# Performance work log

Measured on AMD Instinct MI355X. Metric: run time of the kernel, lower is better.

The kernel has to match this reference:

```python
import jax, jax.numpy as jnp
import numpy as np

HEADS = 8
DIM_HEAD = 64
NB_FEATURES = 256
CHUNK = 128          # chunk size used by performer's causal_linear_attention_noncuda
EPS_KERNEL = 1e-4    # eps in softmax_kernel feature map
EPS_DENOM = 1e-6     # eps added to k_cumsum in the denominator


def softmax_kernel(data, proj, is_query):
    # FAVOR+ positive softmax random features (performer_pytorch.softmax_kernel)
    # data: [B,H,N,D], proj: [M,D]
    d = data.shape[-1]
    normalizer = d ** -0.25
    ratio = proj.shape[0] ** -0.5
    data_dash = jnp.einsum('bhnd,md->bhnm', data * normalizer, proj)
    # ||x||^2 / (2*sqrt(d))
    diag = jnp.sum(data * data, axis=-1, keepdims=True) * 0.5 * (normalizer ** 2)
    if is_query:
        m = jax.lax.stop_gradient(jnp.max(data_dash, axis=-1, keepdims=True))
    else:
        m = jax.lax.stop_gradient(jnp.max(data_dash, axis=(-1, -2), keepdims=True))
    return ratio * (jnp.exp(data_dash - diag - m) + EPS_KERNEL)


def causal_linear_attention(qp, kp, v, chunk=CHUNK):
    # Chunked causal linear attention (O(N) in seq len):
    # out_i = q'_i . S_i / (q'_i . z_i), S_i = sum_{j<=i} k'_j v_j^T, z_i = cumsum k'_j
    B, H, N, M = qp.shape
    E = v.shape[-1]
    C = N // chunk

    def to_chunks(x):
        return x.reshape(B, H, C, chunk, x.shape[-1]).transpose(2, 0, 1, 3, 4)

    qc, kc, vc = to_chunks(qp), to_chunks(kp), to_chunks(v)
    k0 = jnp.zeros((B, H, M), qp.dtype)
    s0 = jnp.zeros((B, H, M, E), qp.dtype)

    def step(carry, inp):
        k_last, s_last = carry
        q, k, vv = inp  # [B,H,c,M], [B,H,c,M], [B,H,c,E]
        k_cum = k_last[:, :, None, :] + jnp.cumsum(k, axis=2)           # [B,H,c,M]
        d_inv = 1.0 / jnp.einsum('bhnm,bhnm->bhn', q, k_cum + EPS_DENOM)
        ctx = jnp.einsum('bhnm,bhne->bhnme', k, vv)                      # [B,H,c,M,E]
        s_cum = s_last[:, :, None] + jnp.cumsum(ctx, axis=2)             # [B,H,c,M,E]
        out = jnp.einsum('bhnme,bhnm,bhn->bhne', s_cum, q, d_inv)        # [B,H,c,E]
        return (k_cum[:, :, -1, :], s_cum[:, :, -1]), out

    _, outs = jax.lax.scan(step, (k0, s0), (qc, kc, vc))  # [C,B,H,c,E]
    return outs.transpose(1, 2, 0, 3, 4).reshape(B, H, N, E)


def setup_inputs() -> dict:
    key = jax.random.key(0)
    k1, k2, k3, k4 = jax.random.split(key, 4)
    B, N, D = 4, 2048, 512
    return {
        'query': jax.random.normal(k1, (B, N, D), jnp.float32),
        'key': jax.random.normal(k2, (B, N, D), jnp.float32),
        'value': jax.random.normal(k3, (B, N, D), jnp.float32),
        'projection': jax.random.normal(k4, (NB_FEATURES, DIM_HEAD), jnp.float32),
    }


def reference(query, key, value, projection):
    B, N, D = query.shape

    def split(x):  # [B,N,D] -> [B,H,N,Dh]
        return x.reshape(B, N, HEADS, DIM_HEAD).transpose(0, 2, 1, 3)

    q, k, v = split(query), split(key), split(value)
    qp = softmax_kernel(q, projection, is_query=True)
    kp = softmax_kernel(k, projection, is_query=False)
    out = causal_linear_attention(qp, kp, v)
    return out.transpose(0, 2, 1, 3).reshape(B, N, D)
```

## Files before the change

### kernel.cpp

```cpp
#include <hip/hip_runtime.h>
#include <math.h>

#define BB 4
#define NN 2048
#define DD 512
#define HH 8
#define DH 64
#define MM 256
#define BH 32
#define CHK 128
#define NCH 16
#define ROWS (BH*NN)

constexpr float NRM   = 0.35355339059327373f;
constexpr float RATIO = 0.0625f;
constexpr float EPSK  = 1e-4f;
constexpr float EPSD  = 1e-6f;
constexpr float REPS  = 0.0625f * 1e-4f;

#define OFFB_QP   ((size_t)0)
#define OFFB_SP   ((size_t)33554432)
#define OFFB_KP   (OFFB_SP + (size_t)16777216)
#define OFFB_VT   (OFFB_KP + (size_t)33554432)
#define OFFB_Z    (OFFB_VT + (size_t)8388608)
#define OFFB_KMP  (OFFB_Z  + (size_t)524288)
#define OFFB_SF   (OFFB_KMP + (size_t)4096)
#define OFFB_PJB  (OFFB_SF + (size_t)4096)

typedef __attribute__((ext_vector_type(8))) short short8;
typedef __attribute__((ext_vector_type(4))) float f32x4;

__device__ __forceinline__ float b2f(ushort u) {
  union { float f; unsigned int i; } x; x.i = ((unsigned int)u) << 16; return x.f;
}
__device__ __forceinline__ ushort f2b(float f) {
  unsigned int u = __float_as_uint(f);
  unsigned int r = (u + 0x7FFFu + ((u >> 16) & 1u)) >> 16;
  return (ushort)r;
}

#define MFMA(a,b,c) __builtin_amdgcn_mfma_f32_16x16x32_bf16(a, b, c, 0, 0, 0)

__global__ __launch_bounds__(256) void prep_kernel(const float* __restrict__ proj,
                                                   char* __restrict__ ws) {
  const int i = blockIdx.x*256 + threadIdx.x;
  float4 v = *(const float4*)(proj + (size_t)i*4);
  ushort4 o;
  o.x = f2b(v.x); o.y = f2b(v.y); o.z = f2b(v.z); o.w = f2b(v.w);
  *(ushort4*)((ushort*)(ws + OFFB_PJB) + (size_t)i*4) = o;
}

template<int MODE>
__device__ __forceinline__ void featm_body(const float* __restrict__ inp,
                                           const ushort* __restrict__ projb,
                                           char* __restrict__ ws,
                                           char* lds, int blk) {
  ushort* xh = (ushort*)lds;
  ushort* xl = xh + 64*72;
  ushort* ps = xl + 64*72;
  ushort* qt = (ushort*)lds;
  float* diag_s = (float*)(lds + 36864);
  float (*wmax)[4] = (float(*)[4])(lds + 37120);
  float* kred = (float*)(lds + 38144);

  const int t  = threadIdx.x;
  const int w  = t >> 6;
  const int l  = t & 63;
  const int lq = l >> 4;
  const int ln = l & 15;

  const int rowbase = blk * 64;
  const int bh = rowbase >> 11;
  const int b  = bh >> 3, h = bh & 7;
  const int n0 = rowbase & (NN - 1);

  {
    const int r  = t >> 2;
    const int c0 = (t & 3) * 16;
    const float* src = inp + ((size_t)(b*NN + n0 + r))*DD + h*DH + c0;
    float vv[16];
    #pragma unroll
    for (int j = 0; j < 4; ++j) {
      float4 v = *(const float4*)(src + j*4);
      vv[4*j+0] = v.x*NRM; vv[4*j+1] = v.y*NRM;
      vv[4*j+2] = v.z*NRM; vv[4*j+3] = v.w*NRM;
    }
    float s = 0.f;
    ushort hi[16], lo[16];
    #pragma unroll
    for (int j = 0; j < 16; ++j) {
      s += vv[j]*vv[j];
      hi[j] = f2b(vv[j]);
      lo[j] = f2b(vv[j] - b2f(hi[j]));
    }
    *(short8*)(xh + r*72 + c0)     = *(short8*)&hi[0];
    *(short8*)(xh + r*72 + c0 + 8) = *(short8*)&hi[8];
    *(short8*)(xl + r*72 + c0)     = *(short8*)&lo[0];
    *(short8*)(xl + r*72 + c0 + 8) = *(short8*)&lo[8];
    s += __shfl_xor(s, 1); s += __shfl_xor(s, 2);
    if ((t & 3) == 0) diag_s[r] = 0.5f * s;
  }

  f32x4 acc[4][4];
  #pragma unroll
  for (int mt = 0; mt < 4; ++mt)
    #pragma unroll
    for (int c = 0; c < 4; ++c) acc[mt][c] = (f32x4){0.f,0.f,0.f,0.f};

  #pragma unroll
  for (int p = 0; p < 2; ++p) {
    if (p) __syncthreads();
    #pragma unroll
    for (int ld = 0; ld < 4; ++ld) {
      int flat = t + 256*ld;
      int r = flat >> 3, g = flat & 7;
      *(short8*)(ps + r*72 + g*8) = *(const short8*)(projb + (size_t)(p*128 + r)*DH + g*8);
    }
    __syncthreads();
    #pragma unroll
    for (int kk = 0; kk < 2; ++kk) {
      short8 ah[4], al[4];
      #pragma unroll
      for (int mt = 0; mt < 4; ++mt) {
        ah[mt] = *(const short8*)(xh + (mt*16 + ln)*72 + kk*32 + lq*8);
        al[mt] = *(const short8*)(xl + (mt*16 + ln)*72 + kk*32 + lq*8);
      }
      #pragma unroll
      for (int ntl = 0; ntl < 2; ++ntl) {
        short8 bf = *(const short8*)(ps + (w*32 + ntl*16 + ln)*72 + kk*32 + lq*8);
        #pragma unroll
        for (int mt = 0; mt < 4; ++mt) {
          acc[mt][2*p+ntl] = MFMA(al[mt], bf, acc[mt][2*p+ntl]);
          acc[mt][2*p+ntl] = MFMA(ah[mt], bf, acc[mt][2*p+ntl]);
        }
      }
    }
  }

  if (MODE == 0) {
    #pragma unroll
    for (int mt = 0; mt < 4; ++mt)
      #pragma unroll
      for (int reg = 0; reg < 4; ++reg) {
        float m = acc[mt][0][reg];
        #pragma unroll
        for (int c = 1; c < 4; ++c) m = fmaxf(m, acc[mt][c][reg]);
        m = fmaxf(m, __shfl_xor(m, 1));
        m = fmaxf(m, __shfl_xor(m, 2));
        m = fmaxf(m, __shfl_xor(m, 4));
        m = fmaxf(m, __shfl_xor(m, 8));
        if (ln == 0) wmax[mt*16 + lq*4 + reg][w] = m;
      }
  } else {
    float mx = -1e30f;
    #pragma unroll
    for (int mt = 0; mt < 4; ++mt)
      #pragma unroll
      for (int c = 0; c < 4; ++c)
        #pragma unroll
        for (int reg = 0; reg < 4; ++reg) mx = fmaxf(mx, acc[mt][c][reg]);
    #pragma unroll
    for (int m = 1; m < 64; m <<= 1) mx = fmaxf(mx, __shfl_xor(mx, m));
    if (l == 0) kred[w] = mx;
  }
  __syncthreads();

  float km = 0.f;
  if (MODE == 1) {
    km = fmaxf(fmaxf(kred[0], kred[1]), fmaxf(kred[2], kred[3]));
    if (t == 0) ((float*)(ws + OFFB_KMP))[blk] = km;
  }

  #pragma unroll
  for (int mt = 0; mt < 4; ++mt)
    #pragma unroll
    for (int reg = 0; reg < 4; ++reg) {
      const int row = mt*16 + lq*4 + reg;
      float rm;
      if (MODE == 0) {
        float4 wm4 = *(const float4*)&wmax[row][0];
        rm = fmaxf(fmaxf(wm4.x, wm4.y), fmaxf(wm4.z, wm4.w));
      } else {
        rm = km;
      }
      const float dg = diag_s[row];
      #pragma unroll
      for (int c = 0; c < 4; ++c) {
        const int f = (c >> 1)*128 + w*32 + (c & 1)*16 + ln;
        const float e = __expf(acc[mt][c][reg] - dg - rm);
        qt[row*264 + f] = f2b(MODE == 0 ? RATIO*(e + EPSK) : e);
      }
    }
  __syncthreads();

  ushort* dstbase = (ushort*)(ws + (MODE == 0 ? OFFB_QP : OFFB_KP)) + (size_t)rowbase*MM;
  #pragma unroll
  for (int ld = 0; ld < 8; ++ld) {
    int flat = t + 256*ld;
    int row = flat >> 5, g = flat & 31;
    *(short8*)(dstbase + (size_t)row*MM + g*8) = *(const short8*)(qt + row*264 + g*8);
  }
}

__device__ __forceinline__ void vt_body(const float* __restrict__ value,
                                        char* __restrict__ ws,
                                        char* lds, int blk) {
  float (*vsh)[68] = (float(*)[68])lds;
  const int t = threadIdx.x;
  const int bh = blk >> 4, nc = blk & 15;
  const int b = bh >> 3, h = bh & 7;
  const int n0 = nc * CHK;
  #pragma unroll
  for (int l = 0; l < 8; ++l) {
    int flat = t + 256*l;
    int r = flat >> 4, g = flat & 15;
    *(float4*)&vsh[r][g*4] = *(const float4*)(value + ((size_t)(b*NN + n0 + r))*DD + h*DH + g*4);
  }
  __syncthreads();
  const int e = t & 63, qd = t >> 6;
  ushort* vt = (ushort*)(ws + OFFB_VT) + ((size_t)bh*DH + e)*NN + n0 + qd*32;
  #pragma unroll
  for (int p = 0; p < 16; ++p) {
    unsigned int lo = f2b(vsh[qd*32 + 2*p][e]);
    unsigned int hi = f2b(vsh[qd*32 + 2*p + 1][e]);
    ((unsigned int*)vt)[p] = lo | (hi << 16);
  }
}

__global__ __launch_bounds__(256) void mega_kernel(const float* __restrict__ q,
                                                   const float* __restrict__ k,
                                                   const float* __restrict__ v,
                                                   char* __restrict__ ws) {
  __shared__ __align__(16) char lds[38160];
  const ushort* projb = (const ushort*)(ws + OFFB_PJB);
  const int blk = blockIdx.x;
  if (blk < 1024)       featm_body<0>(q, projb, ws, lds, blk);
  else if (blk < 2048)  featm_body<1>(k, projb, ws, lds, blk - 1024);
  else                  vt_body(v, ws, lds, blk - 2048);
}

__global__ __launch_bounds__(256) void sfac_kernel(char* __restrict__ ws) {
  const int blk = blockIdx.x*256 + threadIdx.x;
  const int bh = blk >> 5;
  const float* kmp = (const float*)(ws + OFFB_KMP);
  float km = -1e30f;
  #pragma unroll
  for (int i = 0; i < 32; ++i) km = fmaxf(km, kmp[bh*32 + i]);
  ((float*)(ws + OFFB_SF))[blk] = RATIO * __expf(kmp[blk] - km);
}

__global__ __launch_bounds__(256) void sprefix_kernel(char* __restrict__ ws) {
  __shared__ __align__(16) unsigned int kpTu[16*68];
  __shared__ __align__(16) ushort Vts[64*136];
  __shared__ float zred[16][16];

  const int t  = threadIdx.x;
  const int w  = t >> 6;
  const int l  = t & 63;
  const int lq = l >> 4;
  const int ln = l & 15;
  const int bh = blockIdx.x >> 4;
  const int ms = blockIdx.x & 15;

  const ushort* kpb = (const ushort*)(ws + OFFB_KP) + (size_t)bh*NN*MM + ms*16;
  const ushort* vtb = (const ushort*)(ws + OFFB_VT) + (size_t)bh*DH*NN;
  const float*  sf  = (const float*)(ws + OFFB_SF);
  ushort* spb = (ushort*)(ws + OFFB_SP) + (size_t)bh*NCH*DH*MM + ms*16;
  float*  zb  = (float*)(ws + OFFB_Z) + (size_t)bh*NCH*MM + ms*16;

  f32x4 acc = (f32x4){0.f,0.f,0.f,0.f};
  float zrun = 0.f;

  for (int tc = 0; tc < NCH; ++tc) {
    __syncthreads();

    if (t < 16) {
      if (tc > 0) {
        float s = 0.f;
        #pragma unroll
        for (int q = 0; q < 16; ++q) s += zred[q][t];
        zrun += s;
      }
      zb[(size_t)tc*MM + t] = zrun;
    }
    {
      ushort* sp = spb + (size_t)tc*DH*MM;
      #pragma unroll
      for (int reg = 0; reg < 4; ++reg)
        sp[(size_t)(w*16 + lq*4 + reg)*MM + ln] = f2b(acc[reg]);
    }

    const ushort* kslice = kpb + (size_t)tc*CHK*MM;
    if (t < 128) {
      int jp = t >> 1, mo = t & 1;
      float s0 = sf[bh*32 + tc*2 + (jp >> 5)];
      short8 a = *(const short8*)(kslice + (size_t)(2*jp)*MM + mo*8);
      short8 c = *(const short8*)(kslice + (size_t)(2*jp+1)*MM + mo*8);
      #pragma unroll
      for (int i = 0; i < 8; ++i) {
        ushort ua = f2b(fmaf(b2f((ushort)a[i]), s0, REPS));
        ushort uc = f2b(fmaf(b2f((ushort)c[i]), s0, REPS));
        kpTu[(mo*8 + i)*68 + jp] = (unsigned int)ua | ((unsigned int)uc << 16);
      }
    }
    #pragma unroll
    for (int it = 0; it < 4; ++it) {
      int slot = t + 256*it;
      int e = slot >> 4, g = slot & 15;
      *(short8*)(Vts + e*136 + g*8) = *(const short8*)(vtb + (size_t)e*NN + tc*CHK + g*8);
    }
    __syncthreads();

    {
      int m = t & 15, q = t >> 4;
      float s = 0.f;
      #pragma unroll
      for (int u = 0; u < 4; ++u) {
        unsigned int p = kpTu[m*68 + q*4 + u];
        s += b2f((ushort)(p & 0xFFFF)) + b2f((ushort)(p >> 16));
      }
      zred[q][m] = s;
    }

    #pragma unroll
    for (int kk = 0; kk < 4; ++kk) {
      short8 af = *(const short8*)(Vts + (w*16 + ln)*136 + kk*32 + lq*8);
      short8 bf = *(const short8*)((const ushort*)kpTu + (size_t)ln*136 + kk*32 + lq*8);
      acc = MFMA(af, bf, acc);
    }
  }
}

__global__ __launch_bounds__(256) void fused_kernel(float* __restrict__ out,
                                                    char* __restrict__ ws) {
  __shared__ __align__(16) char lds[52224];
  __shared__ float den_i[128];
  __shared__ float dinv_s[128];

  const int t  = threadIdx.x;
  const int w  = t >> 6;
  const int l  = t & 63;
  const int lq = l >> 4;
  const int ln = l & 15;
  const int rt0 = w;
  const int rt1 = 7 - w;
  const int blk = blockIdx.x;
  const int bh = blk >> 4, tc = blk & 15;
  const int b = bh >> 3, h = bh & 7;
  const size_t rowbase = (size_t)bh*NN + tc*CHK;

  const ushort* qpg = (const ushort*)(ws + OFFB_QP) + rowbase*MM;
  const ushort* kpg = (const ushort*)(ws + OFFB_KP) + rowbase*MM;
  const ushort* spg = (const ushort*)(ws + OFFB_SP) + (size_t)blk*DH*MM;
  const float*  sf  = (const float*)(ws + OFFB_SF);
  const float sc0 = sf[blk*2], sc1 = sf[blk*2 + 1];

  ushort* qs = (ushort*)lds;
  ushort* ks = qs + 128*72;
  ushort* ss = ks + 128*72;

  f32x4 acc[2][8];
  #pragma unroll
  for (int mt = 0; mt < 2; ++mt)
    #pragma unroll
    for (int nt = 0; nt < 8; ++nt) acc[mt][nt] = (f32x4){0.f,0.f,0.f,0.f};
  f32x4 oacc[2][4];
  #pragma unroll
  for (int mt = 0; mt < 2; ++mt)
    #pragma unroll
    for (int nt = 0; nt < 4; ++nt) oacc[mt][nt] = (f32x4){0.f,0.f,0.f,0.f};

  for (int mc = 0; mc < 4; ++mc) {
    __syncthreads();
    #pragma unroll
    for (int ld2 = 0; ld2 < 4; ++ld2) {
      int flat = t + 256*ld2; int r = flat >> 3, g = flat & 7;
      *(short8*)(qs + r*72 + g*8) = *(const short8*)(qpg + (size_t)r*MM + mc*64 + g*8);
    }
    #pragma unroll
    for (int ld2 = 0; ld2 < 4; ++ld2) {
      int flat = t + 256*ld2; int r = flat >> 3, g = flat & 7;
      short8 kv = *(const short8*)(kpg + (size_t)r*MM + mc*64 + g*8);
      const float sc = (r & 64) ? sc1 : sc0;
      ushort ov[8];
      #pragma unroll
      for (int i = 0; i < 8; ++i) ov[i] = f2b(fmaf(b2f((ushort)kv[i]), sc, REPS));
      *(short8*)(ks + r*72 + g*8) = *(short8*)&ov[0];
    }
    #pragma unroll
    for (int ld2 = 0; ld2 < 2; ++ld2) {
      int flat = t + 256*ld2; int e = flat >> 3, g = flat & 7;
      *(short8*)(ss + e*72 + g*8) = *(const short8*)(spg + (size_t)e*MM + mc*64 + g*8);
    }
    __syncthreads();
    #pragma unroll
    for (int kk = 0; kk < 2; ++kk) {
      short8 af0 = *(const short8*)(qs + (rt0*16 + ln)*72 + kk*32 + lq*8);
      short8 af1 = *(const short8*)(qs + (rt1*16 + ln)*72 + kk*32 + lq*8);
      #pragma unroll
      for (int nt = 0; nt < 8; ++nt) {
        if (nt <= rt1) {
          short8 bf = *(const short8*)(ks + (nt*16 + ln)*72 + kk*32 + lq*8);
          if (nt <= rt0) acc[0][nt] = MFMA(af0, bf, acc[0][nt]);
          acc[1][nt] = MFMA(af1, bf, acc[1][nt]);
        }
      }
      #pragma unroll
      for (int nt = 0; nt < 4; ++nt) {
        short8 bf = *(const short8*)(ss + (nt*16 + ln)*72 + kk*32 + lq*8);
        oacc[0][nt] = MFMA(af0, bf, oacc[0][nt]);
        oacc[1][nt] = MFMA(af1, bf, oacc[1][nt]);
      }
    }
  }

  __syncthreads();

  ushort* P   = (ushort*)lds;
  ushort* Vts = (ushort*)(lds + 34816);

  float rs[2][4] = {{0,0,0,0},{0,0,0,0}};
  #pragma unroll
  for (int mt = 0; mt < 2; ++mt) {
    const int ibase = (mt ? rt1 : rt0) * 16;
    #pragma unroll
    for (int nt = 0; nt < 8; ++nt)
      #pragma unroll
      for (int reg = 0; reg < 4; ++reg) {
        int i = ibase + lq*4 + reg;
        int j = nt*16 + ln;
        float v = (j <= i) ? acc[mt][nt][reg] : 0.f;
        rs[mt][reg] += v;
        P[i*136 + j] = f2b(v);
      }
  }
  #pragma unroll
  for (int mt = 0; mt < 2; ++mt) {
    const int ibase = (mt ? rt1 : rt0) * 16;
    #pragma unroll
    for (int reg = 0; reg < 4; ++reg) {
      float s = rs[mt][reg];
      s += __shfl_xor(s, 1); s += __shfl_xor(s, 2);
      s += __shfl_xor(s, 4); s += __shfl_xor(s, 8);
      if (ln == 0) den_i[ibase + lq*4 + reg] = s;
    }
  }

  const ushort* vtg = (const ushort*)(ws + OFFB_VT) + (size_t)bh*DH*NN + tc*CHK;
  #pragma unroll
  for (int ld2 = 0; ld2 < 4; ++ld2) {
    int flat = t + 256*ld2; int e = flat >> 4, g = flat & 15;
    *(short8*)(Vts + e*136 + g*8) = *(const short8*)(vtg + (size_t)e*NN + g*8);
  }
  __syncthreads();

  {
    const float* zp = (const float*)(ws + OFFB_Z) + (size_t)blk*MM;
    const int r = t >> 1, hf = t & 1;
    const ushort* qrow = qpg + (size_t)r*MM + hf*128;
    float s = 0.f;
    #pragma unroll
    for (int g = 0; g < 16; ++g) {
      short8 qv = *(const short8*)(qrow + g*8);
      const float* zz = zp + hf*128 + g*8;
      #pragma unroll
      for (int x = 0; x < 8; ++x)
        s += b2f((ushort)qv[x]) * (zz[x] + EPSD);
    }
    s += __shfl_xor(s, 1);
    if (hf == 0) dinv_s[r] = 1.0f / (s + den_i[r]);
  }
  __syncthreads();

  #pragma unroll
  for (int kk = 0; kk < 4; ++kk) {
    short8 af0 = *(const short8*)(P + (rt0*16 + ln)*136 + kk*32 + lq*8);
    short8 af1 = *(const short8*)(P + (rt1*16 + ln)*136 + kk*32 + lq*8);
    #pragma unroll
    for (int nt = 0; nt < 4; ++nt) {
      short8 bf = *(const short8*)(Vts + (nt*16 + ln)*136 + kk*32 + lq*8);
      oacc[0][nt] = MFMA(af0, bf, oacc[0][nt]);
      oacc[1][nt] = MFMA(af1, bf, oacc[1][nt]);
    }
  }

  #pragma unroll
  for (int mt = 0; mt < 2; ++mt) {
    const int ibase = (mt ? rt1 : rt0) * 16;
    #pragma unroll
    for (int reg = 0; reg < 4; ++reg) {
      const int i = ibase + lq*4 + reg;
      const float di = dinv_s[i];
      float* dst = out + ((size_t)(b*NN) + tc*CHK + i)*DD + h*DH;
      #pragma unroll
      for (int nt = 0; nt < 4; ++nt)
        dst[nt*16 + ln] = oacc[mt][nt][reg] * di;
    }
  }
}

extern "C" void kernel_launch(void* const* d_in, const int* in_sizes, int n_in,
                              void* d_out, int out_size, void* d_ws, size_t ws_size,
                              hipStream_t stream) {
  (void)in_sizes; (void)n_in; (void)out_size; (void)ws_size;
  const float* q    = (const float*)d_in[0];
  const float* k    = (const float*)d_in[1];
  const float* v    = (const float*)d_in[2];
  const float* proj = (const float*)d_in[3];
  float* out = (float*)d_out;
  char*  ws  = (char*)d_ws;

  prep_kernel<<<16, 256, 0, stream>>>(proj, ws);
  mega_kernel<<<2560, 256, 0, stream>>>(q, k, v, ws);
  sfac_kernel<<<4, 256, 0, stream>>>(ws);
  sprefix_kernel<<<512, 256, 0, stream>>>(ws);
  fused_kernel<<<512, 256, 0, stream>>>(out, ws);
}
```

Before: 187.9 us.

## Fuse Q and K feature maps into one block and drop bf16 hi/lo split

Each block now computes both the query and key FAVOR+ feature maps for the same 64 rows. The projection tile loaded into LDS is shared across both, and the grid shrinks from 2560 to 1536 blocks. The split-bf16 (hi+lo) emulation of the projection matmul is removed, so each product is a single bf16 MFMA, halving MFMA work and LDS traffic. The cost is lower precision in the projection logits, which feed exp(), and higher register pressure from holding two accumulator sets.

Result: slower. 201.3 us (+7.2%).

```diff
diff --git a/kernel.cpp b/kernel.cpp
--- a/kernel.cpp
+++ b/kernel.cpp
@@ -50,18 +50,19 @@
   *(ushort4*)((ushort*)(ws + OFFB_PJB) + (size_t)i*4) = o;
 }
 
-template<int MODE>
-__device__ __forceinline__ void featm_body(const float* __restrict__ inp,
-                                           const ushort* __restrict__ projb,
-                                           char* __restrict__ ws,
-                                           char* lds, int blk) {
-  ushort* xh = (ushort*)lds;
-  ushort* xl = xh + 64*72;
-  ushort* ps = xl + 64*72;
+__device__ __forceinline__ void featqk_body(const float* __restrict__ qin,
+                                            const float* __restrict__ kin,
+                                            const ushort* __restrict__ projb,
+                                            char* __restrict__ ws,
+                                            char* lds, int blk) {
+  ushort* xq = (ushort*)lds;
+  ushort* xk = xq + 64*72;
+  ushort* ps = xk + 64*72;
   ushort* qt = (ushort*)lds;
-  float* diag_s = (float*)(lds + 36864);
-  float (*wmax)[4] = (float(*)[4])(lds + 37120);
-  float* kred = (float*)(lds + 38144);
+  float* diag_q = (float*)(lds + 36864);
+  float* diag_k = (float*)(lds + 37120);
+  float (*wmax)[4] = (float(*)[4])(lds + 37376);
+  float* kred = (float*)(lds + 38400);
 
   const int t  = threadIdx.x;
   const int w  = t >> 6;
@@ -77,35 +78,40 @@
   {
     const int r  = t >> 2;
     const int c0 = (t & 3) * 16;
-    const float* src = inp + ((size_t)(b*NN + n0 + r))*DD + h*DH + c0;
-    float vv[16];
+    const size_t off = ((size_t)(b*NN + n0 + r))*DD + h*DH + c0;
+    const float* srcq = qin + off;
+    const float* srck = kin + off;
+    float sq = 0.f, sk = 0.f;
+    ushort hq[16], hk[16];
     #pragma unroll
     for (int j = 0; j < 4; ++j) {
-      float4 v = *(const float4*)(src + j*4);
-      vv[4*j+0] = v.x*NRM; vv[4*j+1] = v.y*NRM;
-      vv[4*j+2] = v.z*NRM; vv[4*j+3] = v.w*NRM;
-    }
-    float s = 0.f;
-    ushort hi[16], lo[16];
-    #pragma unroll
-    for (int j = 0; j < 16; ++j) {
-      s += vv[j]*vv[j];
-      hi[j] = f2b(vv[j]);
-      lo[j] = f2b(vv[j] - b2f(hi[j]));
-    }
-    *(short8*)(xh + r*72 + c0)     = *(short8*)&hi[0];
-    *(short8*)(xh + r*72 + c0 + 8) = *(short8*)&hi[8];
-    *(short8*)(xl + r*72 + c0)     = *(short8*)&lo[0];
-    *(short8*)(xl + r*72 + c0 + 8) = *(short8*)&lo[8];
-    s += __shfl_xor(s, 1); s += __shfl_xor(s, 2);
-    if ((t & 3) == 0) diag_s[r] = 0.5f * s;
-  }
-
-  f32x4 acc[4][4];
+      float4 vq = *(const float4*)(srcq + j*4);
+      float4 vk = *(const float4*)(srck + j*4);
+      float aq[4] = {vq.x*NRM, vq.y*NRM, vq.z*NRM, vq.w*NRM};
+      float ak[4] = {vk.x*NRM, vk.y*NRM, vk.z*NRM, vk.w*NRM};
+      #pragma unroll
+      for (int x = 0; x < 4; ++x) {
+        sq += aq[x]*aq[x]; sk += ak[x]*ak[x];
+        hq[4*j+x] = f2b(aq[x]); hk[4*j+x] = f2b(ak[x]);
+      }
+    }
+    *(short8*)(xq + r*72 + c0)     = *(short8*)&hq[0];
+    *(short8*)(xq + r*72 + c0 + 8) = *(short8*)&hq[8];
+    *(short8*)(xk + r*72 + c0)     = *(short8*)&hk[0];
+    *(short8*)(xk + r*72 + c0 + 8) = *(short8*)&hk[8];
+    sq += __shfl_xor(sq, 1); sq += __shfl_xor(sq, 2);
+    sk += __shfl_xor(sk, 1); sk += __shfl_xor(sk, 2);
+    if ((t & 3) == 0) { diag_q[r] = 0.5f*sq; diag_k[r] = 0.5f*sk; }
+  }
+
+  f32x4 accq[4][4], acck[4][4];
   #pragma unroll
   for (int mt = 0; mt < 4; ++mt)
     #pragma unroll
-    for (int c = 0; c < 4; ++c) acc[mt][c] = (f32x4){0.f,0.f,0.f,0.f};
+    for (int c = 0; c < 4; ++c) {
+      accq[mt][c] = (f32x4){0.f,0.f,0.f,0.f};
+      acck[mt][c] = (f32x4){0.f,0.f,0.f,0.f};
+    }
 
   #pragma unroll
   for (int p = 0; p < 2; ++p) {
@@ -119,86 +125,101 @@
     __syncthreads();
     #pragma unroll
     for (int kk = 0; kk < 2; ++kk) {
-      short8 ah[4], al[4];
+      short8 aq[4], ak[4];
       #pragma unroll
       for (int mt = 0; mt < 4; ++mt) {
-        ah[mt] = *(const short8*)(xh + (mt*16 + ln)*72 + kk*32 + lq*8);
-        al[mt] = *(const short8*)(xl + (mt*16 + ln)*72 + kk*32 + lq*8);
+        aq[mt] = *(const short8*)(xq + (mt*16 + ln)*72 + kk*32 + lq*8);
+        ak[mt] = *(const short8*)(xk + (mt*16 + ln)*72 + kk*32 + lq*8);
       }
       #pragma unroll
       for (int ntl = 0; ntl < 2; ++ntl) {
         short8 bf = *(const short8*)(ps + (w*32 + ntl*16 + ln)*72 + kk*32 + lq*8);
         #pragma unroll
         for (int mt = 0; mt < 4; ++mt) {
-          acc[mt][2*p+ntl] = MFMA(al[mt], bf, acc[mt][2*p+ntl]);
-          acc[mt][2*p+ntl] = MFMA(ah[mt], bf, acc[mt][2*p+ntl]);
+          accq[mt][2*p+ntl] = MFMA(aq[mt], bf, accq[mt][2*p+ntl]);
+          acck[mt][2*p+ntl] = MFMA(ak[mt], bf, acck[mt][2*p+ntl]);
         }
       }
     }
   }
 
-  if (MODE == 0) {
-    #pragma unroll
-    for (int mt = 0; mt < 4; ++mt)
-      #pragma unroll
-      for (int reg = 0; reg < 4; ++reg) {
-        float m = acc[mt][0][reg];
-        #pragma unroll
-        for (int c = 1; c < 4; ++c) m = fmaxf(m, acc[mt][c][reg]);
-        m = fmaxf(m, __shfl_xor(m, 1));
-        m = fmaxf(m, __shfl_xor(m, 2));
-        m = fmaxf(m, __shfl_xor(m, 4));
-        m = fmaxf(m, __shfl_xor(m, 8));
-        if (ln == 0) wmax[mt*16 + lq*4 + reg][w] = m;
-      }
-  } else {
+  #pragma unroll
+  for (int mt = 0; mt < 4; ++mt)
+    #pragma unroll
+    for (int reg = 0; reg < 4; ++reg) {
+      float m = accq[mt][0][reg];
+      #pragma unroll
+      for (int c = 1; c < 4; ++c) m = fmaxf(m, accq[mt][c][reg]);
+      m = fmaxf(m, __shfl_xor(m, 1));
+      m = fmaxf(m, __shfl_xor(m, 2));
+      m = fmaxf(m, __shfl_xor(m, 4));
+      m = fmaxf(m, __shfl_xor(m, 8));
+      if (ln == 0) wmax[mt*16 + lq*4 + reg][w] = m;
+    }
+  {
     float mx = -1e30f;
     #pragma unroll
     for (int mt = 0; mt < 4; ++mt)
       #pragma unroll
       for (int c = 0; c < 4; ++c)
         #pragma unroll
-        for (int reg = 0; reg < 4; ++reg) mx = fmaxf(mx, acc[mt][c][reg]);
+        for (int reg = 0; reg < 4; ++reg) mx = fmaxf(mx, acck[mt][c][reg]);
     #pragma unroll
     for (int m = 1; m < 64; m <<= 1) mx = fmaxf(mx, __shfl_xor(mx, m));
     if (l == 0) kred[w] = mx;
   }
   __syncthreads();
 
-  float km = 0.f;
-  if (MODE == 1) {
-    km = fmaxf(fmaxf(kred[0], kred[1]), fmaxf(kred[2], kred[3]));
-    if (t == 0) ((float*)(ws + OFFB_KMP))[blk] = km;
-  }
+  const float km = fmaxf(fmaxf(kred[0], kred[1]), fmaxf(kred[2], kred[3]));
+  if (t == 0) ((float*)(ws + OFFB_KMP))[blk] = km;
 
   #pragma unroll
   for (int mt = 0; mt < 4; ++mt)
     #pragma unroll
     for (int reg = 0; reg < 4; ++reg) {
       const int row = mt*16 + lq*4 + reg;
-      float rm;
-      if (MODE == 0) {
-        float4 wm4 = *(const float4*)&wmax[row][0];
-        rm = fmaxf(fmaxf(wm4.x, wm4.y), fmaxf(wm4.z, wm4.w));
-      } else {
-        rm = km;
-      }
-      const float dg = diag_s[row];
+      float4 wm4 = *(const float4*)&wmax[row][0];
+      const float rm = fmaxf(fmaxf(wm4.x, wm4.y), fmaxf(wm4.z, wm4.w));
+      const float dg = diag_q[row];
       #pragma unroll
       for (int c = 0; c < 4; ++c) {
         const int f = (c >> 1)*128 + w*32 + (c & 1)*16 + ln;
-        const float e = __expf(acc[mt][c][reg] - dg - rm);
-        qt[row*264 + f] = f2b(MODE == 0 ? RATIO*(e + EPSK) : e);
-      }
-    }
-  __syncthreads();
-
-  ushort* dstbase = (ushort*)(ws + (MODE == 0 ? OFFB_QP : OFFB_KP)) + (size_t)rowbase*MM;
-  #pragma unroll
-  for (int ld = 0; ld < 8; ++ld) {
-    int flat = t + 256*ld;
-    int row = flat >> 5, g = flat & 31;
-    *(short8*)(dstbase + (size_t)row*MM + g*8) = *(const short8*)(qt + row*264 + g*8);
+        qt[row*264 + f] = f2b(RATIO*(__expf(accq[mt][c][reg] - dg - rm) + EPSK));
+      }
+    }
+  __syncthreads();
+  {
+    ushort* dstbase = (ushort*)(ws + OFFB_QP) + (size_t)rowbase*MM;
+    #pragma unroll
+    for (int ld = 0; ld < 8; ++ld) {
+      int flat = t + 256*ld;
+      int row = flat >> 5, g = flat & 31;
+      *(short8*)(dstbase + (size_t)row*MM + g*8) = *(const short8*)(qt + row*264 + g*8);
+    }
+  }
+  __syncthreads();
+
+  #pragma unroll
+  for (int mt = 0; mt < 4; ++mt)
+    #pragma unroll
+    for (int reg = 0; reg < 4; ++reg) {
+      const int row = mt*16 + lq*4 + reg;
+      const float dg = diag_k[row];
+      #pragma unroll
+      for (int c = 0; c < 4; ++c) {
+        const int f = (c >> 1)*128 + w*32 + (c & 1)*16 + ln;
+        qt[row*264 + f] = f2b(__expf(acck[mt][c][reg] - dg - km));
+      }
+    }
+  __syncthreads();
+  {
+    ushort* dstbase = (ushort*)(ws + OFFB_KP) + (size_t)rowbase*MM;
+    #pragma unroll
+    for (int ld = 0; ld < 8; ++ld) {
+      int flat = t + 256*ld;
+      int row = flat >> 5, g = flat & 31;
+      *(short8*)(dstbase + (size_t)row*MM + g*8) = *(const short8*)(qt + row*264 + g*8);
+    }
   }
 }
 
@@ -231,12 +252,11 @@
                                                    const float* __restrict__ k,
                                                    const float* __restrict__ v,
                                                    char* __restrict__ ws) {
-  __shared__ __align__(16) char lds[38160];
+  __shared__ __align__(16) char lds[38416];
   const ushort* projb = (const ushort*)(ws + OFFB_PJB);
   const int blk = blockIdx.x;
-  if (blk < 1024)       featm_body<0>(q, projb, ws, lds, blk);
-  else if (blk < 2048)  featm_body<1>(k, projb, ws, lds, blk - 1024);
-  else                  vt_body(v, ws, lds, blk - 2048);
+  if (blk < 1024) featqk_body(q, k, projb, ws, lds, blk);
+  else            vt_body(v, ws, lds, blk - 1024);
 }
 
 __global__ __launch_bounds__(256) void sfac_kernel(char* __restrict__ ws) {
@@ -511,7 +531,7 @@
   char*  ws  = (char*)d_ws;
 
   prep_kernel<<<16, 256, 0, stream>>>(proj, ws);
-  mega_kernel<<<2560, 256, 0, stream>>>(q, k, v, ws);
+  mega_kernel<<<1536, 256, 0, stream>>>(q, k, v, ws);
   sfac_kernel<<<4, 256, 0, stream>>>(ws);
   sprefix_kernel<<<512, 256, 0, stream>>>(ws);
   fused_kernel<<<512, 256, 0, stream>>>(out, ws);
```
